# Kernel optimization log

Measured on AMD Instinct MI355X. Metric: run time of the kernel, lower is better.

The kernel has to match this reference:

```python
import jax, jax.numpy as jnp
import numpy as np

R = 3                 # search_radius
S2 = (2 * R + 1) ** 2  # 49 correlation channels
VIS_PIXEL_SCALE = 0.1  # arcsec / pixel


def _interp_tokens(tokens, sh, sw, dh, dw):
    # tokens [B, N, D] on (sh, sw) grid -> (dh, dw) grid
    B, N, D = tokens.shape
    x = jnp.transpose(tokens, (0, 2, 1)).reshape(B, D, sh, sw)
    if (sh, sw) != (dh, dw):
        # torch F.interpolate bilinear align_corners=False == jax half-pixel bilinear
        x = jax.image.resize(x, (B, D, dh, dw), method='bilinear')
    return x  # [B, D, dh, dw]


def _l2norm(x, eps=1e-12):
    n = jnp.sqrt(jnp.sum(x * x, axis=1, keepdims=True))
    return x / jnp.maximum(n, eps)


def _corr_volume(q, ref):
    # q, ref: [B, D, H, W]; local cosine-similarity volume [B, S2, H, W]
    q = _l2norm(q)
    ref = _l2norm(ref)
    B, D, H, W = q.shape
    refp = jnp.pad(ref, ((0, 0), (0, 0), (R, R), (R, R)), mode='edge')  # replicate pad
    slices = [
        jnp.sum(q * jax.lax.dynamic_slice(refp, (0, 0, R + dy, R + dx), (B, D, H, W)), axis=1)
        for dy in range(-R, R + 1) for dx in range(-R, R + 1)
    ]
    return jnp.stack(slices, axis=1)


def _conv5(x, w, b):
    y = jax.lax.conv_general_dilated(x, w, (1, 1), 'SAME',
                                     dimension_numbers=('NCHW', 'OIHW', 'NCHW'))
    return y + b[None, :, None, None]


def _refine_net(x, w0, b0, w1, b1, w2, b2):
    h = jax.nn.gelu(_conv5(x, w0, b0), approximate=False)
    h = jax.nn.gelu(_conv5(h, w1, b1), approximate=False)
    return _conv5(h, w2, b2)


def setup_inputs() -> dict:
    key = jax.random.key(0)
    ks = jax.random.split(key, 8)
    B, D = 4, 256
    rubin_tokens = jax.random.normal(ks[0], (B, 64 * 64, D), dtype=jnp.float32)
    vis_tokens = jax.random.normal(ks[1], (B, 128 * 128, D), dtype=jnp.float32)
    in_ch = 2 + S2 + 1  # 52
    hid = 32
    def kaiming(k, shape):
        fan_in = shape[1] * shape[2] * shape[3]
        return jax.random.normal(k, shape, dtype=jnp.float32) / np.sqrt(fan_in)
    w0 = kaiming(ks[2], (hid, in_ch, 5, 5)); b0 = jnp.zeros((hid,), jnp.float32)
    w1 = kaiming(ks[3], (hid, hid, 5, 5));   b1 = jnp.zeros((hid,), jnp.float32)
    w2 = kaiming(ks[4], (2, hid, 5, 5));     b2 = jnp.zeros((2,), jnp.float32)
    log_temp = jnp.asarray(np.log(0.1), dtype=jnp.float32)
    return {
        'rubin_tokens': rubin_tokens, 'vis_tokens': vis_tokens,
        'w0': w0, 'b0': b0, 'w1': w1, 'b1': b1, 'w2': w2, 'b2': b2,
        'log_temp': log_temp,
        'rubin_h': 64, 'rubin_w': 64, 'vis_h': 128, 'vis_w': 128,
        'img_h': 2048, 'img_w': 2048,
    }


def reference(rubin_tokens, vis_tokens, w0, b0, w1, b1, w2, b2, log_temp,
              rubin_h, rubin_w, vis_h, vis_w, img_h, img_w):
    Hc, Wc = max(rubin_h, vis_h), max(rubin_w, vis_w)
    q = _interp_tokens(rubin_tokens, rubin_h, rubin_w, Hc, Wc)  # [B,D,Hc,Wc]
    k = _interp_tokens(vis_tokens, vis_h, vis_w, Hc, Wc)
    corr = _corr_volume(q, k)  # [B,S2,Hc,Wc]

    # soft-argmax over the (2R+1)^2 neighborhood
    coords = jnp.arange(-R, R + 1, dtype=corr.dtype)
    cy, cx = jnp.meshgrid(coords, coords, indexing='ij')
    cy = cy.reshape(1, S2, 1, 1)
    cx = cx.reshape(1, S2, 1, 1)
    temp = jnp.exp(log_temp)
    weights = jax.nn.softmax(corr / temp, axis=1)
    dy = jnp.sum(weights * cy, axis=1, keepdims=True)
    dx = jnp.sum(weights * cx, axis=1, keepdims=True)
    confidence = jnp.max(weights, axis=1, keepdims=True)
    raw_offsets = jnp.concatenate([dy, dx], axis=1)  # [B,2,Hc,Wc]

    x = jnp.concatenate([raw_offsets, corr, confidence], axis=1)  # [B,52,Hc,Wc]
    residual = _refine_net(x, w0, b0, w1, b1, w2, b2)
    refined = raw_offsets + residual

    sky_per_token_y = img_h * VIS_PIXEL_SCALE / Hc
    sky_per_token_x = img_w * VIS_PIXEL_SCALE / Wc
    dra = refined[:, 1:2] * sky_per_token_x
    ddec = refined[:, 0:1] * sky_per_token_y
    # [B,5,Hc,Wc]: dra, ddec, raw_dy, raw_dx, confidence
    return jnp.concatenate([dra, ddec, dy, dx, confidence], axis=1)
```

## Files before the change

kernel.cpp:

```cpp
#include <hip/hip_runtime.h>
#include <math.h>

#define Hh 128
#define Ww 128
#define Dd 256
#define Bb 4
#define HW (Hh*Ww)
#define NPIX (Bb*HW)
#define WP 132

typedef __attribute__((ext_vector_type(8))) short s16x8;
typedef __attribute__((ext_vector_type(4))) float f32x4;

__device__ __forceinline__ unsigned short f2bf(float f) {
    unsigned u = __float_as_uint(f);
    u += 0x7FFF + ((u >> 16) & 1);
    return (unsigned short)(u >> 16);
}

__device__ __forceinline__ float gelu_exact(float v) {
    return 0.5f * v * (1.0f + erff(v * 0.70710678118654752f));
}

#define ZGRAN 1115136
__global__ __launch_bounds__(256) void setup_fill(const float* __restrict__ w0,
                                                  const float* __restrict__ w1,
                                                  const float* __restrict__ w2,
                                                  unsigned short* __restrict__ wb0,
                                                  unsigned short* __restrict__ wb1,
                                                  unsigned short* __restrict__ wb2,
                                                  uint4* __restrict__ zbase) {
    int t = blockIdx.x * 256 + threadIdx.x;
    if (t < ZGRAN) {
        zbase[t] = (uint4){0, 0, 0, 0};
        return;
    }
    int u = t - ZGRAN;
    if (u < 51200) {
        int tap = u >> 11; int r = u & 2047; int n = r >> 6; int k = r & 63;
        wb0[u] = (k < 52) ? f2bf(w0[n * 1300 + k * 25 + tap]) : (unsigned short)0;
    } else if (u < 76800) {
        int v = u - 51200; int tap = v >> 10; int r = v & 1023; int n = r >> 5; int k = r & 31;
        wb1[v] = f2bf(w1[n * 800 + k * 25 + tap]);
    } else if (u < 89600) {
        int v = u - 76800; int tap = v >> 9; int r = v & 511; int n = r >> 5; int k = r & 31;
        wb2[v] = (n < 2) ? f2bf(w2[n * 800 + k * 25 + tap]) : (unsigned short)0;
    }
}

__global__ __launch_bounds__(256) void norm_fused(const float* __restrict__ vis,
                                                  const float* __restrict__ rub,
                                                  unsigned short* __restrict__ kn,
                                                  unsigned short* __restrict__ qn) {
    int tid = threadIdx.x;
    int g16 = tid >> 4, l = tid & 15;
    int blk = blockIdx.x;
    if (blk < 4096) {
        int pix = blk * 16 + g16;
        const float* base = vis + (size_t)pix * Dd + l * 4;
        float4 v[4];
#pragma unroll
        for (int i = 0; i < 4; i++) v[i] = *(const float4*)(base + i * 64);
        float ss = 0.f;
#pragma unroll
        for (int i = 0; i < 4; i++)
            ss += v[i].x * v[i].x + v[i].y * v[i].y + v[i].z * v[i].z + v[i].w * v[i].w;
#pragma unroll
        for (int o = 1; o <= 8; o <<= 1) ss += __shfl_xor(ss, o, 64);
        float inv = __builtin_amdgcn_rsqf(fmaxf(ss, 1e-24f));
        unsigned short* op = kn + (size_t)pix * Dd + l * 4;
#pragma unroll
        for (int i = 0; i < 4; i++) {
            ushort4 o4;
            o4.x = f2bf(v[i].x * inv); o4.y = f2bf(v[i].y * inv);
            o4.z = f2bf(v[i].z * inv); o4.w = f2bf(v[i].w * inv);
            *(ushort4*)(op + i * 64) = o4;
        }
    } else {
        int pix = (blk - 4096) * 16 + g16;
        int b = pix >> 14; int yx = pix & 16383; int y = yx >> 7; int x = yx & 127;
        float sy = 0.5f * y - 0.25f;
        float sx = 0.5f * x - 0.25f;
        int y0 = (int)floorf(sy); float fy = sy - (float)y0;
        int x0 = (int)floorf(sx); float fx = sx - (float)x0;
        int y0c = max(y0, 0), y1c = min(y0 + 1, 63);
        int x0c = max(x0, 0), x1c = min(x0 + 1, 63);
        const float* base = rub + (size_t)b * 4096 * Dd + l * 4;
        const float* p00 = base + (size_t)(y0c * 64 + x0c) * Dd;
        const float* p01 = base + (size_t)(y0c * 64 + x1c) * Dd;
        const float* p10 = base + (size_t)(y1c * 64 + x0c) * Dd;
        const float* p11 = base + (size_t)(y1c * 64 + x1c) * Dd;
        float w00 = (1.f - fy) * (1.f - fx), w01 = (1.f - fy) * fx;
        float w10 = fy * (1.f - fx), w11 = fy * fx;
        float4 bv[4];
        float ss = 0.f;
#pragma unroll
        for (int i = 0; i < 4; i++) {
            float4 a = *(const float4*)(p00 + i * 64);
            float4 b1 = *(const float4*)(p01 + i * 64);
            float4 c = *(const float4*)(p10 + i * 64);
            float4 d = *(const float4*)(p11 + i * 64);
            float4 v;
            v.x = w00 * a.x + w01 * b1.x + w10 * c.x + w11 * d.x;
            v.y = w00 * a.y + w01 * b1.y + w10 * c.y + w11 * d.y;
            v.z = w00 * a.z + w01 * b1.z + w10 * c.z + w11 * d.z;
            v.w = w00 * a.w + w01 * b1.w + w10 * c.w + w11 * d.w;
            bv[i] = v;
            ss += v.x * v.x + v.y * v.y + v.z * v.z + v.w * v.w;
        }
#pragma unroll
        for (int o = 1; o <= 8; o <<= 1) ss += __shfl_xor(ss, o, 64);
        float inv = __builtin_amdgcn_rsqf(fmaxf(ss, 1e-24f));
        unsigned short* op = qn + (size_t)pix * Dd + l * 4;
#pragma unroll
        for (int i = 0; i < 4; i++) {
            ushort4 o4;
            o4.x = f2bf(bv[i].x * inv); o4.y = f2bf(bv[i].y * inv);
            o4.z = f2bf(bv[i].z * inv); o4.w = f2bf(bv[i].w * inv);
            *(ushort4*)(op + i * 64) = o4;
        }
    }
}

__global__ __launch_bounds__(1024) void corr_block(const unsigned short* __restrict__ qn,
                                                   const unsigned short* __restrict__ kn,
                                                   const float* __restrict__ log_temp,
                                                   unsigned short* __restrict__ xb,
                                                   float* __restrict__ out) {
    __shared__ char smem[484 * 5 * 16];
    int tid = threadIdx.x;
    int wid = tid >> 6, lane = tid & 63, l15 = lane & 15, quad = lane >> 4;
    int blk = blockIdx.x;
    int b = blk >> 6, rem = blk & 63;
    int y0 = ((rem >> 3) & 7) << 4, x0 = (rem & 7) << 4;
    int y = y0 + wid;

    const unsigned short* src0; int dst0;
    const unsigned short* src1 = nullptr; int dst1 = 0;
    bool hav1;
    {
        int g = tid;
        int px = g >> 2, sub = g & 3;
        int ry = px / 22, rx = px - ry * 22;
        int yy = min(max(y0 - 3 + ry, 0), 127);
        int xx = min(max(x0 - 3 + rx, 0), 127);
        src0 = kn + ((size_t)(b << 14) + yy * 128 + xx) * 256 + sub * 8;
        dst0 = (px * 5 + sub) * 16;
        g = 1024 + tid;
        hav1 = (g < 1936);
        int gc = hav1 ? g : 1935;
        px = gc >> 2; sub = gc & 3;
        ry = px / 22; rx = px - ry * 22;
        yy = min(max(y0 - 3 + ry, 0), 127);
        xx = min(max(x0 - 3 + rx, 0), 127);
        src1 = kn + ((size_t)(b << 14) + yy * 128 + xx) * 256 + sub * 8;
        dst1 = (px * 5 + sub) * 16;
    }
    int lpixoff[10];
#pragma unroll
    for (int f = 0; f < 10; f++) {
        int p = min(f * 16 + l15, 153);
        int pr = p / 22, pc = p - pr * 22;
        lpixoff[f] = (((wid + pr) * 22 + pc) * 5 + quad) * 16;
    }
    const unsigned short* aptr = qn + ((size_t)(b << 14) + y * 128 + x0 + l15) * 256 + quad * 8;

    f32x4 acc[10];
#pragma unroll
    for (int f = 0; f < 10; f++) acc[f] = (f32x4){0.f, 0.f, 0.f, 0.f};

    uint4 v0 = *(const uint4*)src0;
    uint4 v1 = *(const uint4*)src1;
    s16x8 an = *(const s16x8*)aptr;
    for (int c = 0; c < 8; c++) {
        uint4 w0v = v0, w1v = v1;
        s16x8 a = an;
        if (c < 7) {
            v0 = *(const uint4*)(src0 + (c + 1) * 32);
            v1 = *(const uint4*)(src1 + (c + 1) * 32);
            an = *(const s16x8*)(aptr + (c + 1) * 32);
        }
        __syncthreads();
        *(uint4*)(smem + dst0) = w0v;
        if (hav1) *(uint4*)(smem + dst1) = w1v;
        __syncthreads();
#pragma unroll
        for (int f = 0; f < 10; f++) {
            s16x8 bf = *(const s16x8*)(smem + lpixoff[f]);
            acc[f] = __builtin_amdgcn_mfma_f32_16x16x32_bf16(a, bf, acc[f], 0, 0, 0);
        }
    }

    float inv_temp = expf(-log_temp[0]);
    float vmax[4] = {-1e30f, -1e30f, -1e30f, -1e30f};
#pragma unroll
    for (int f = 0; f < 10; f++) {
        int n = f * 16 + l15;
        if (n <= 153) {
            int dy = n / 22 - 3;
            int rx = n - (dy + 3) * 22;
#pragma unroll
            for (int i = 0; i < 4; i++) {
                int m = quad * 4 + i;
                int dx = rx - m - 3;
                if ((unsigned)(dx + 3) <= 6u) vmax[i] = fmaxf(vmax[i], acc[f][i]);
            }
        }
    }
#pragma unroll
    for (int o = 1; o <= 8; o <<= 1) {
#pragma unroll
        for (int i = 0; i < 4; i++) vmax[i] = fmaxf(vmax[i], __shfl_xor(vmax[i], o, 64));
    }
    float se[4] = {0, 0, 0, 0}, sey[4] = {0, 0, 0, 0}, sex[4] = {0, 0, 0, 0}, emax[4] = {0, 0, 0, 0};
    unsigned short* xrow = xb + ((size_t)(b * WP + y + 2) * WP + x0 + 2) * 64;
#pragma unroll
    for (int f = 0; f < 10; f++) {
        int n = f * 16 + l15;
        if (n <= 153) {
            int dy = n / 22 - 3;
            int rx = n - (dy + 3) * 22;
#pragma unroll
            for (int i = 0; i < 4; i++) {
                int m = quad * 4 + i;
                int dx = rx - m - 3;
                if ((unsigned)(dx + 3) <= 6u) {
                    float v = acc[f][i];
                    float e = expf((v - vmax[i]) * inv_temp);
                    se[i] += e;
                    sey[i] += e * (float)dy;
                    sex[i] += e * (float)dx;
                    emax[i] = fmaxf(emax[i], e);
                    xrow[(size_t)m * 64 + 2 + (dy + 3) * 7 + (dx + 3)] = f2bf(v);
                }
            }
        }
    }
#pragma unroll
    for (int o = 1; o <= 8; o <<= 1) {
#pragma unroll
        for (int i = 0; i < 4; i++) {
            se[i] += __shfl_xor(se[i], o, 64);
            sey[i] += __shfl_xor(sey[i], o, 64);
            sex[i] += __shfl_xor(sex[i], o, 64);
            emax[i] = fmaxf(emax[i], __shfl_xor(emax[i], o, 64));
        }
    }
    if (l15 == 0) {
#pragma unroll
        for (int i = 0; i < 4; i++) {
            int m = quad * 4 + i;
            float inv_se = 1.0f / se[i];
            float dyv = sey[i] * inv_se, dxv = sex[i] * inv_se, conf = emax[i] * inv_se;
            unsigned short* xp = xrow + (size_t)m * 64;
            xp[0] = f2bf(dyv); xp[1] = f2bf(dxv); xp[51] = f2bf(conf);
            float* op = out + (size_t)b * 5 * HW + y * 128 + x0 + m;
            op[2 * HW] = dyv; op[3 * HW] = dxv; op[4 * HW] = conf;
        }
    }
}

template <int KS, int OC, bool GELU>
__global__ __launch_bounds__(1024) void conv_tile(const unsigned short* __restrict__ in,
                                                  const unsigned short* __restrict__ wb,
                                                  const float* __restrict__ bias,
                                                  unsigned short* __restrict__ outp) {
    constexpr int ICP = KS * 32;
    constexpr int NF = OC / 16;
    constexpr int ABYTES = 400 * 5 * 16;
    constexpr int WBYTES = 5 * OC * 5 * 16;
    __shared__ char smem[ABYTES + WBYTES];
    int tid = threadIdx.x;
    int wv = tid >> 6, lane = tid & 63, l15 = lane & 15, quad = lane >> 4;
    int blk = blockIdx.x;
    int b = blk >> 6, ty = (blk >> 3) & 7, tx = blk & 7;
    int y0 = ty * 16, x0 = tx * 16;

    f32x4 acc[NF];
#pragma unroll
    for (int g = 0; g < NF; g++) acc[g] = (f32x4){0.f, 0.f, 0.f, 0.f};

    for (int ks = 0; ks < KS; ks++) {
        __syncthreads();
#pragma unroll
        for (int i = 0; i < 2; i++) {
            int g = i * 1024 + tid;
            if (g < 1600) {
                int px = g >> 2, sub = g & 3;
                int r = px / 20, c = px - r * 20;
                *(uint4*)(smem + (px * 5 + sub) * 16) =
                    *(const uint4*)(in + ((size_t)(b * WP + y0 + r) * WP + x0 + c) * ICP + ks * 32 + sub * 8);
            }
        }
        for (int ky = 0; ky < 5; ky++) {
            if (ky > 0) __syncthreads();
            constexpr int WGR = 5 * OC * 4;
#pragma unroll
            for (int i = 0; i < (WGR + 1023) / 1024; i++) {
                int g = i * 1024 + tid;
                if (g < WGR) {
                    int nl = g >> 2, sub = g & 3;
                    *(uint4*)(smem + ABYTES + (nl * 5 + sub) * 16) =
                        *(const uint4*)(wb + ((size_t)(ky * 5 * OC) + nl) * ICP + ks * 32 + sub * 8);
                }
            }
            __syncthreads();
#pragma unroll
            for (int kx = 0; kx < 5; kx++) {
                int abyte = (((wv + ky) * 20 + l15 + kx) * 5 + quad) * 16;
                s16x8 a = *(const s16x8*)(smem + abyte);
#pragma unroll
                for (int g = 0; g < NF; g++) {
                    int wbyte = ABYTES + ((kx * OC + g * 16 + l15) * 5 + quad) * 16;
                    s16x8 bf = *(const s16x8*)(smem + wbyte);
                    acc[g] = __builtin_amdgcn_mfma_f32_16x16x32_bf16(a, bf, acc[g], 0, 0, 0);
                }
            }
        }
    }
    size_t orow = ((size_t)(b * WP + y0 + wv + 2) * WP + x0 + 2) * OC;
#pragma unroll
    for (int g = 0; g < NF; g++) {
        float bv = bias[g * 16 + l15];
#pragma unroll
        for (int r = 0; r < 4; r++) {
            int m = quad * 4 + r;
            float v = acc[g][r] + bv;
            if (GELU) v = gelu_exact(v);
            outp[orow + (size_t)m * OC + g * 16 + l15] = f2bf(v);
        }
    }
}

__global__ __launch_bounds__(1024) void conv_final_tile(const unsigned short* __restrict__ in,
                                                        const unsigned short* __restrict__ wb,
                                                        const float* __restrict__ bias,
                                                        float* __restrict__ out) {
    constexpr int ICP = 32, OC = 16;
    constexpr int ABYTES = 400 * 5 * 16;
    constexpr int WBYTES = 5 * OC * 5 * 16;
    __shared__ char smem[ABYTES + WBYTES];
    int tid = threadIdx.x;
    int wv = tid >> 6, lane = tid & 63, l15 = lane & 15, quad = lane >> 4;
    int blk = blockIdx.x;
    int b = blk >> 6, ty = (blk >> 3) & 7, tx = blk & 7;
    int y0 = ty * 16, x0 = tx * 16;

    f32x4 acc = (f32x4){0.f, 0.f, 0.f, 0.f};
    __syncthreads();
#pragma unroll
    for (int i = 0; i < 2; i++) {
        int g = i * 1024 + tid;
        if (g < 1600) {
            int px = g >> 2, sub = g & 3;
            int r = px / 20, c = px - r * 20;
            *(uint4*)(smem + (px * 5 + sub) * 16) =
                *(const uint4*)(in + ((size_t)(b * WP + y0 + r) * WP + x0 + c) * ICP + sub * 8);
        }
    }
    for (int ky = 0; ky < 5; ky++) {
        if (ky > 0) __syncthreads();
        constexpr int WGR = 5 * OC * 4;
        {
            int g = tid;
            if (g < WGR) {
                int nl = g >> 2, sub = g & 3;
                *(uint4*)(smem + ABYTES + (nl * 5 + sub) * 16) =
                    *(const uint4*)(wb + ((size_t)(ky * 5 * OC) + nl) * ICP + sub * 8);
            }
        }
        __syncthreads();
#pragma unroll
        for (int kx = 0; kx < 5; kx++) {
            int abyte = (((wv + ky) * 20 + l15 + kx) * 5 + quad) * 16;
            s16x8 a = *(const s16x8*)(smem + abyte);
            int wbyte = ABYTES + ((kx * OC + l15) * 5 + quad) * 16;
            s16x8 bf = *(const s16x8*)(smem + wbyte);
            acc = __builtin_amdgcn_mfma_f32_16x16x32_bf16(a, bf, acc, 0, 0, 0);
        }
    }
    if (l15 < 2) {
        float bv = bias[l15];
#pragma unroll
        for (int r = 0; r < 4; r++) {
            int m = quad * 4 + r;
            size_t p5 = (size_t)b * 5 * HW + (y0 + wv) * Ww + x0 + m;
            float a = acc[r] + bv;
            if (l15 == 0) {
                float dyv = out[p5 + 2 * HW];
                out[p5 + HW] = (dyv + a) * 1.6f;
            } else {
                float dxv = out[p5 + 3 * HW];
                out[p5] = (dxv + a) * 1.6f;
            }
        }
    }
}

extern "C" void kernel_launch(void* const* d_in, const int* in_sizes, int n_in,
                              void* d_out, int out_size, void* d_ws, size_t ws_size,
                              hipStream_t stream) {
    const float* rub = (const float*)d_in[0];
    const float* vis = (const float*)d_in[1];
    const float* w0 = (const float*)d_in[2];
    const float* b0 = (const float*)d_in[3];
    const float* w1 = (const float*)d_in[4];
    const float* b1 = (const float*)d_in[5];
    const float* w2 = (const float*)d_in[6];
    const float* b2 = (const float*)d_in[7];
    const float* log_temp = (const float*)d_in[8];
    float* out = (float*)d_out;

    char* ws = (char*)d_ws;
    size_t off = 0;
    const size_t PADPIX = (size_t)Bb * WP * WP;
    unsigned short* kn = (unsigned short*)(ws + off); off += (size_t)NPIX * Dd * 2;
    unsigned short* qn = (unsigned short*)(ws + off); off += (size_t)NPIX * Dd * 2;
    unsigned short* xbp = (unsigned short*)(ws + off); off += PADPIX * 64 * 2;
    unsigned short* h1p = (unsigned short*)(ws + off); off += PADPIX * 32 * 2;
    unsigned short* h2p = (unsigned short*)(ws + off); off += PADPIX * 32 * 2;
    unsigned short* wb0 = (unsigned short*)(ws + off); off += 51200 * 2;
    unsigned short* wb1 = (unsigned short*)(ws + off); off += 25600 * 2;
    unsigned short* wb2 = (unsigned short*)(ws + off); off += 12800 * 2;

    setup_fill<<<4706, 256, 0, stream>>>(w0, w1, w2, wb0, wb1, wb2, (uint4*)xbp);
    norm_fused<<<8192, 256, 0, stream>>>(vis, rub, kn, qn);
    corr_block<<<256, 1024, 0, stream>>>(qn, kn, log_temp, xbp, out);
    conv_tile<2, 32, true><<<256, 1024, 0, stream>>>(xbp, wb0, b0, h1p);
    conv_tile<1, 32, true><<<256, 1024, 0, stream>>>(h1p, wb1, b1, h2p);
    conv_final_tile<<<256, 1024, 0, stream>>>(h2p, wb2, b2, out);
}
```

Baseline: 214.4 us.

## Halve tile height and block size to double block count, add two-row register blocking

Corr and conv kernels now use 16x8 pixel tiles with 512- or 256-thread blocks, so the grid grows from 256 to 512 blocks. The intent is better CU fill on a many-CU GPU and more resident blocks per CU, given the new launch bounds and smaller shared memory. Conv waves now compute two output rows each, sharing each loaded weight fragment across two MFMAs. Blocks are ordered so neighbouring blocks interleave batch and x-halves. The trade-off is more halo overhead per output pixel, since smaller tiles reload more redundant border data.

Measured after the change: 258.2 us. 20.4% more time.

```diff
diff --git a/kernel.cpp b/kernel.cpp
--- a/kernel.cpp
+++ b/kernel.cpp
@@ -122,39 +122,33 @@
     }
 }
 
-__global__ __launch_bounds__(1024) void corr_block(const unsigned short* __restrict__ qn,
-                                                   const unsigned short* __restrict__ kn,
-                                                   const float* __restrict__ log_temp,
-                                                   unsigned short* __restrict__ xb,
-                                                   float* __restrict__ out) {
-    __shared__ char smem[484 * 5 * 16];
+__global__ __launch_bounds__(512, 4) void corr_block(const unsigned short* __restrict__ qn,
+                                                     const unsigned short* __restrict__ kn,
+                                                     const float* __restrict__ log_temp,
+                                                     unsigned short* __restrict__ xb,
+                                                     float* __restrict__ out) {
+    __shared__ char smem[308 * 5 * 16];
     int tid = threadIdx.x;
     int wid = tid >> 6, lane = tid & 63, l15 = lane & 15, quad = lane >> 4;
     int blk = blockIdx.x;
-    int b = blk >> 6, rem = blk & 63;
-    int y0 = ((rem >> 3) & 7) << 4, x0 = (rem & 7) << 4;
+    int r = blk & 7, t = blk >> 3;
+    int b = r >> 1, xh = r & 1;
+    int ty = t & 15, txl = t >> 4;
+    int y0 = ty * 8, x0 = (xh * 4 + txl) * 16;
     int y = y0 + wid;
 
-    const unsigned short* src0; int dst0;
-    const unsigned short* src1 = nullptr; int dst1 = 0;
-    bool hav1;
-    {
-        int g = tid;
-        int px = g >> 2, sub = g & 3;
+    const unsigned short* srcs[3]; int dsts[3]; bool have[3];
+#pragma unroll
+    for (int s = 0; s < 3; s++) {
+        int g = s * 512 + tid;
+        have[s] = (g < 1232);
+        int gc = have[s] ? g : 1231;
+        int px = gc >> 2, sub = gc & 3;
         int ry = px / 22, rx = px - ry * 22;
         int yy = min(max(y0 - 3 + ry, 0), 127);
         int xx = min(max(x0 - 3 + rx, 0), 127);
-        src0 = kn + ((size_t)(b << 14) + yy * 128 + xx) * 256 + sub * 8;
-        dst0 = (px * 5 + sub) * 16;
-        g = 1024 + tid;
-        hav1 = (g < 1936);
-        int gc = hav1 ? g : 1935;
-        px = gc >> 2; sub = gc & 3;
-        ry = px / 22; rx = px - ry * 22;
-        yy = min(max(y0 - 3 + ry, 0), 127);
-        xx = min(max(x0 - 3 + rx, 0), 127);
-        src1 = kn + ((size_t)(b << 14) + yy * 128 + xx) * 256 + sub * 8;
-        dst1 = (px * 5 + sub) * 16;
+        srcs[s] = kn + ((size_t)(b << 14) + yy * 128 + xx) * 256 + sub * 8;
+        dsts[s] = (px * 5 + sub) * 16;
     }
     int lpixoff[10];
 #pragma unroll
@@ -169,20 +163,24 @@
 #pragma unroll
     for (int f = 0; f < 10; f++) acc[f] = (f32x4){0.f, 0.f, 0.f, 0.f};
 
-    uint4 v0 = *(const uint4*)src0;
-    uint4 v1 = *(const uint4*)src1;
+    uint4 v[3];
+#pragma unroll
+    for (int s = 0; s < 3; s++) v[s] = *(const uint4*)srcs[s];
     s16x8 an = *(const s16x8*)aptr;
     for (int c = 0; c < 8; c++) {
-        uint4 w0v = v0, w1v = v1;
+        uint4 w[3];
+#pragma unroll
+        for (int s = 0; s < 3; s++) w[s] = v[s];
         s16x8 a = an;
         if (c < 7) {
-            v0 = *(const uint4*)(src0 + (c + 1) * 32);
-            v1 = *(const uint4*)(src1 + (c + 1) * 32);
+#pragma unroll
+            for (int s = 0; s < 3; s++) v[s] = *(const uint4*)(srcs[s] + (c + 1) * 32);
             an = *(const s16x8*)(aptr + (c + 1) * 32);
         }
         __syncthreads();
-        *(uint4*)(smem + dst0) = w0v;
-        if (hav1) *(uint4*)(smem + dst1) = w1v;
+#pragma unroll
+        for (int s = 0; s < 3; s++)
+            if (have[s]) *(uint4*)(smem + dsts[s]) = w[s];
         __syncthreads();
 #pragma unroll
         for (int f = 0; f < 10; f++) {
@@ -225,13 +223,13 @@
                 int m = quad * 4 + i;
                 int dx = rx - m - 3;
                 if ((unsigned)(dx + 3) <= 6u) {
-                    float v = acc[f][i];
-                    float e = expf((v - vmax[i]) * inv_temp);
+                    float vv = acc[f][i];
+                    float e = expf((vv - vmax[i]) * inv_temp);
                     se[i] += e;
                     sey[i] += e * (float)dy;
                     sex[i] += e * (float)dx;
                     emax[i] = fmaxf(emax[i], e);
-                    xrow[(size_t)m * 64 + 2 + (dy + 3) * 7 + (dx + 3)] = f2bf(v);
+                    xrow[(size_t)m * 64 + 2 + (dy + 3) * 7 + (dx + 3)] = f2bf(vv);
                 }
             }
         }
@@ -261,43 +259,47 @@
 }
 
 template <int KS, int OC, bool GELU>
-__global__ __launch_bounds__(1024) void conv_tile(const unsigned short* __restrict__ in,
-                                                  const unsigned short* __restrict__ wb,
-                                                  const float* __restrict__ bias,
-                                                  unsigned short* __restrict__ outp) {
+__global__ __launch_bounds__(256, 4) void conv_tile(const unsigned short* __restrict__ in,
+                                                    const unsigned short* __restrict__ wb,
+                                                    const float* __restrict__ bias,
+                                                    unsigned short* __restrict__ outp) {
     constexpr int ICP = KS * 32;
     constexpr int NF = OC / 16;
-    constexpr int ABYTES = 400 * 5 * 16;
+    constexpr int ABYTES = 240 * 5 * 16;
     constexpr int WBYTES = 5 * OC * 5 * 16;
     __shared__ char smem[ABYTES + WBYTES];
     int tid = threadIdx.x;
     int wv = tid >> 6, lane = tid & 63, l15 = lane & 15, quad = lane >> 4;
     int blk = blockIdx.x;
-    int b = blk >> 6, ty = (blk >> 3) & 7, tx = blk & 7;
-    int y0 = ty * 16, x0 = tx * 16;
-
-    f32x4 acc[NF];
-#pragma unroll
-    for (int g = 0; g < NF; g++) acc[g] = (f32x4){0.f, 0.f, 0.f, 0.f};
+    int r = blk & 7, t = blk >> 3;
+    int b = r >> 1, xh = r & 1;
+    int ty = t & 15, txl = t >> 4;
+    int y0 = ty * 8, x0 = (xh * 4 + txl) * 16;
+
+    f32x4 acc[2][NF];
+#pragma unroll
+    for (int rr = 0; rr < 2; rr++)
+#pragma unroll
+        for (int g = 0; g < NF; g++) acc[rr][g] = (f32x4){0.f, 0.f, 0.f, 0.f};
 
     for (int ks = 0; ks < KS; ks++) {
         __syncthreads();
 #pragma unroll
-        for (int i = 0; i < 2; i++) {
-            int g = i * 1024 + tid;
-            if (g < 1600) {
+        for (int i = 0; i < 4; i++) {
+            int g = i * 256 + tid;
+            if (g < 960) {
                 int px = g >> 2, sub = g & 3;
-                int r = px / 20, c = px - r * 20;
+                int rw = px / 20, cc = px - rw * 20;
                 *(uint4*)(smem + (px * 5 + sub) * 16) =
-                    *(const uint4*)(in + ((size_t)(b * WP + y0 + r) * WP + x0 + c) * ICP + ks * 32 + sub * 8);
+                    *(const uint4*)(in + ((size_t)(b * WP + y0 + rw) * WP + x0 + cc) * ICP + ks * 32 + sub * 8);
             }
         }
         for (int ky = 0; ky < 5; ky++) {
             if (ky > 0) __syncthreads();
             constexpr int WGR = 5 * OC * 4;
 #pragma unroll
-            for (int i = 0; i < (WGR + 1023) / 1024; i++) {
-                int g = i * 1024 + tid;
+            for (int i = 0; i < (WGR + 255) / 256; i++) {
+                int g = i * 256 + tid;
                 if (g < WGR) {
                     int nl = g >> 2, sub = g & 3;
                     *(uint4*)(smem + ABYTES + (nl * 5 + sub) * 16) =
@@ -307,62 +309,69 @@
             __syncthreads();
 #pragma unroll
             for (int kx = 0; kx < 5; kx++) {
-                int abyte = (((wv + ky) * 20 + l15 + kx) * 5 + quad) * 16;
-                s16x8 a = *(const s16x8*)(smem + abyte);
+                s16x8 a0 = *(const s16x8*)(smem + (((2 * wv + 0 + ky) * 20 + l15 + kx) * 5 + quad) * 16);
+                s16x8 a1 = *(const s16x8*)(smem + (((2 * wv + 1 + ky) * 20 + l15 + kx) * 5 + quad) * 16);
 #pragma unroll
                 for (int g = 0; g < NF; g++) {
-                    int wbyte = ABYTES + ((kx * OC + g * 16 + l15) * 5 + quad) * 16;
-                    s16x8 bf = *(const s16x8*)(smem + wbyte);
-                    acc[g] = __builtin_amdgcn_mfma_f32_16x16x32_bf16(a, bf, acc[g], 0, 0, 0);
+                    s16x8 bf = *(const s16x8*)(smem + ABYTES + ((kx * OC + g * 16 + l15) * 5 + quad) * 16);
+                    acc[0][g] = __builtin_amdgcn_mfma_f32_16x16x32_bf16(a0, bf, acc[0][g], 0, 0, 0);
+                    acc[1][g] = __builtin_amdgcn_mfma_f32_16x16x32_bf16(a1, bf, acc[1][g], 0, 0, 0);
                 }
             }
         }
     }
-    size_t orow = ((size_t)(b * WP + y0 + wv + 2) * WP + x0 + 2) * OC;
-#pragma unroll
-    for (int g = 0; g < NF; g++) {
-        float bv = bias[g * 16 + l15];
-#pragma unroll
-        for (int r = 0; r < 4; r++) {
-            int m = quad * 4 + r;
-            float v = acc[g][r] + bv;
-            if (GELU) v = gelu_exact(v);
-            outp[orow + (size_t)m * OC + g * 16 + l15] = f2bf(v);
-        }
-    }
-}
-
-__global__ __launch_bounds__(1024) void conv_final_tile(const unsigned short* __restrict__ in,
-                                                        const unsigned short* __restrict__ wb,
-                                                        const float* __restrict__ bias,
-                                                        float* __restrict__ out) {
+#pragma unroll
+    for (int rr = 0; rr < 2; rr++) {
+        size_t orow = ((size_t)(b * WP + y0 + 2 * wv + rr + 2) * WP + x0 + 2) * OC;
+#pragma unroll
+        for (int g = 0; g < NF; g++) {
+            float bv = bias[g * 16 + l15];
+#pragma unroll
+            for (int r4 = 0; r4 < 4; r4++) {
+                int m = quad * 4 + r4;
+                float vv = acc[rr][g][r4] + bv;
+                if (GELU) vv = gelu_exact(vv);
+                outp[orow + (size_t)m * OC + g * 16 + l15] = f2bf(vv);
+            }
+        }
+    }
+}
+
+__global__ __launch_bounds__(256, 4) void conv_final_tile(const unsigned short* __restrict__ in,
+                                                          const unsigned short* __restrict__ wb,
+                                                          const float* __restrict__ bias,
+                                                          float* __restrict__ out) {
     constexpr int ICP = 32, OC = 16;
-    constexpr int ABYTES = 400 * 5 * 16;
+    constexpr int ABYTES = 240 * 5 * 16;
     constexpr int WBYTES = 5 * OC * 5 * 16;
     __shared__ char smem[ABYTES + WBYTES];
     int tid = threadIdx.x;
     int wv = tid >> 6, lane = tid & 63, l15 = lane & 15, quad = lane >> 4;
     int blk = blockIdx.x;
-    int b = blk >> 6, ty = (blk >> 3) & 7, tx = blk & 7;
-    int y0 = ty * 16, x0 = tx * 16;
-
-    f32x4 acc = (f32x4){0.f, 0.f, 0.f, 0.f};
-    __syncthreads();
-#pragma unroll
-    for (int i = 0; i < 2; i++) {
-        int g = i * 1024 + tid;
-        if (g < 1600) {
+    int r = blk & 7, t = blk >> 3;
+    int b = r >> 1, xh = r & 1;
+    int ty = t & 15, txl = t >> 4;
+    int y0 = ty * 8, x0 = (xh * 4 + txl) * 16;
+
+    f32x4 acc[2];
+    acc[0] = (f32x4){0.f, 0.f, 0.f, 0.f};
+    acc[1] = (f32x4){0.f, 0.f, 0.f, 0.f};
+#pragma unroll
+    for (int i = 0; i < 4; i++) {
+        int g = i * 256 + tid;
+        if (g < 960) {
             int px = g >> 2, sub = g & 3;
-            int r = px / 20, c = px - r * 20;
+            int rw = px / 20, cc = px - rw * 20;
             *(uint4*)(smem + (px * 5 + sub) * 16) =
-                *(const uint4*)(in + ((size_t)(b * WP + y0 + r) * WP + x0 + c) * ICP + sub * 8);
+                *(const uint4*)(in + ((size_t)(b * WP + y0 + rw) * WP + x0 + cc) * ICP + sub * 8);
         }
     }
     for (int ky = 0; ky < 5; ky++) {
         if (ky > 0) __syncthreads();
         constexpr int WGR = 5 * OC * 4;
-        {
-            int g = tid;
+#pragma unroll
+        for (int i = 0; i < 2; i++) {
+            int g = i * 256 + tid;
             if (g < WGR) {
                 int nl = g >> 2, sub = g & 3;
                 *(uint4*)(smem + ABYTES + (nl * 5 + sub) * 16) =
@@ -372,26 +381,29 @@
         __syncthreads();
 #pragma unroll
         for (int kx = 0; kx < 5; kx++) {
-            int abyte = (((wv + ky) * 20 + l15 + kx) * 5 + quad) * 16;
-            s16x8 a = *(const s16x8*)(smem + abyte);
-            int wbyte = ABYTES + ((kx * OC + l15) * 5 + quad) * 16;
-            s16x8 bf = *(const s16x8*)(smem + wbyte);
-            acc = __builtin_amdgcn_mfma_f32_16x16x32_bf16(a, bf, acc, 0, 0, 0);
+            s16x8 a0 = *(const s16x8*)(smem + (((2 * wv + 0 + ky) * 20 + l15 + kx) * 5 + quad) * 16);
+            s16x8 a1 = *(const s16x8*)(smem + (((2 * wv + 1 + ky) * 20 + l15 + kx) * 5 + quad) * 16);
+            s16x8 bf = *(const s16x8*)(smem + ABYTES + ((kx * OC + l15) * 5 + quad) * 16);
+            acc[0] = __builtin_amdgcn_mfma_f32_16x16x32_bf16(a0, bf, acc[0], 0, 0, 0);
+            acc[1] = __builtin_amdgcn_mfma_f32_16x16x32_bf16(a1, bf, acc[1], 0, 0, 0);
         }
     }
     if (l15 < 2) {
         float bv = bias[l15];
 #pragma unroll
-        for (int r = 0; r < 4; r++) {
-            int m = quad * 4 + r;
-            size_t p5 = (size_t)b * 5 * HW + (y0 + wv) * Ww + x0 + m;
-            float a = acc[r] + bv;
-            if (l15 == 0) {
-                float dyv = out[p5 + 2 * HW];
-                out[p5 + HW] = (dyv + a) * 1.6f;
-            } else {
-                float dxv = out[p5 + 3 * HW];
-                out[p5] = (dxv + a) * 1.6f;
+        for (int rr = 0; rr < 2; rr++) {
+#pragma unroll
+            for (int r4 = 0; r4 < 4; r4++) {
+                int m = quad * 4 + r4;
+                size_t p5 = (size_t)b * 5 * HW + (y0 + 2 * wv + rr) * Ww + x0 + m;
+                float a = acc[rr][r4] + bv;
+                if (l15 == 0) {
+                    float dyv = out[p5 + 2 * HW];
+                    out[p5 + HW] = (dyv + a) * 1.6f;
+                } else {
+                    float dxv = out[p5 + 3 * HW];
+                    out[p5] = (dxv + a) * 1.6f;
+                }
             }
         }
     }
@@ -425,8 +437,8 @@
 
     setup_fill<<<4706, 256, 0, stream>>>(w0, w1, w2, wb0, wb1, wb2, (uint4*)xbp);
     norm_fused<<<8192, 256, 0, stream>>>(vis, rub, kn, qn);
-    corr_block<<<256, 1024, 0, stream>>>(qn, kn, log_temp, xbp, out);
-    conv_tile<2, 32, true><<<256, 1024, 0, stream>>>(xbp, wb0, b0, h1p);
-    conv_tile<1, 32, true><<<256, 1024, 0, stream>>>(h1p, wb1, b1, h2p);
-    conv_final_tile<<<256, 1024, 0, stream>>>(h2p, wb2, b2, out);
-}
+    corr_block<<<512, 512, 0, stream>>>(qn, kn, log_temp, xbp, out);
+    conv_tile<2, 32, true><<<512, 256, 0, stream>>>(xbp, wb0, b0, h1p);
+    conv_tile<1, 32, true><<<512, 256, 0, stream>>>(h1p, wb1, b1, h2p);
+    conv_final_tile<<<512, 256, 0, stream>>>(h2p, wb2, b2, out);
+}
```
